# Optimization experiments

Measured on AMD Instinct MI355X. Metric: run time of the kernel, lower is better.

## Reference

```python
import jax, jax.numpy as jnp
import numpy as np

N, M, D = 8192, 8192, 64

def setup_inputs() -> dict:
    key = jax.random.key(0)
    kx, ky = jax.random.split(key)
    x = jax.random.normal(kx, (N, D), dtype=jnp.float32)
    y = jax.random.normal(ky, (M, D), dtype=jnp.float32)
    return {"x": x, "y": y}

def reference(x, y):
    T = 1.0
    # Dmat = 2 - euclidean cdist(x, y), computed via the Gram trick.
    sq = (jnp.sum(x * x, axis=1)[:, None]
          + jnp.sum(y * y, axis=1)[None, :]
          - 2.0 * (x @ y.T))
    Dmat = 2.0 - jnp.sqrt(jnp.maximum(sq, 0.0))          # [N, M]
    logprob_rows = jax.nn.log_softmax(Dmat * T, axis=1)   # [N, M]
    logprob_cols = jax.nn.log_softmax(Dmat.T * T, axis=1) # [M, N]
    choice_rows = jnp.argmax(logprob_rows, axis=1)        # [N]
    choice_cols = jnp.argmax(logprob_cols, axis=1)        # [M]
    seq = jnp.arange(M, dtype=choice_cols.dtype)
    mutual = choice_rows[choice_cols] == seq              # [M] bool
    lp_rows = jnp.take_along_axis(logprob_rows, choice_rows[:, None], axis=1)[:, 0]  # [N]
    lp_cols = jnp.take_along_axis(logprob_cols, choice_cols[:, None], axis=1)[:, 0]  # [M]
    # Padded (jit-friendly) form of the boolean compaction: entries where
    # mutual is False are zeroed; mutual mask identifies valid matches.
    log_probs = jnp.where(mutual, lp_rows[choice_cols] + lp_cols, 0.0)  # [M]
    dmatches = jnp.stack([choice_cols, seq], axis=1)      # [M, 2]
    return (log_probs, dmatches, mutual)
```

## Files before the change

kernel.cpp:

```cpp
#include <hip/hip_runtime.h>
#include <stdint.h>

#define NROWS 8192
#define MCOLS 8192
#define DDIM  64

typedef _Float16 half8   __attribute__((ext_vector_type(8)));
typedef float    floatx4 __attribute__((ext_vector_type(4)));

__device__ __forceinline__ unsigned f2key(float f) {
  unsigned u = __float_as_uint(f);
  return (u & 0x80000000u) ? ~u : (u | 0x80000000u);
}
__device__ __forceinline__ float key2f(unsigned k) {
  unsigned u = (k & 0x80000000u) ? (k & 0x7fffffffu) : ~k;
  return __uint_as_float(u);
}

__global__ void convert_kernel(const float* __restrict__ x, const float* __restrict__ y,
                               _Float16* __restrict__ xh, _Float16* __restrict__ xl,
                               _Float16* __restrict__ yh, _Float16* __restrict__ yl,
                               float* __restrict__ xn, float* __restrict__ yn,
                               unsigned long long* __restrict__ rk,
                               unsigned long long* __restrict__ ck,
                               float* __restrict__ rs, float* __restrict__ cs) {
  const int gid  = blockIdx.x * 256 + threadIdx.x;
  if (gid < NROWS) { rk[gid] = 0ull; rs[gid] = 0.0f; ck[gid] = 0ull; cs[gid] = 0.0f; }

  const int row  = gid >> 6;
  const int k    = threadIdx.x & 63;
  const float* src; _Float16 *dh, *dl; float* nout; int r;
  if (row < NROWS) { src = x; dh = xh; dl = xl; nout = xn; r = row; }
  else             { src = y; dh = yh; dl = yl; nout = yn; r = row - NROWS; }

  float f = src[(size_t)r * DDIM + k];
  _Float16 h = (_Float16)f;
  _Float16 l = (_Float16)((f - (float)h) * 2048.0f);
  int pos = ((r >> 4) << 10) + ((k >> 5) << 9) + ((((k >> 3) & 3) << 4) + (r & 15)) * 8 + (k & 7);
  dh[pos] = h;
  dl[pos] = l;

  float s = f * f;
  #pragma unroll
  for (int off = 32; off > 0; off >>= 1) s += __shfl_down(s, off);
  if (k == 0) nout[r] = s;
}

__global__ __launch_bounds__(256, 4) void mfma_tile_kernel(
    const _Float16* __restrict__ xh, const _Float16* __restrict__ xl,
    const _Float16* __restrict__ yh, const _Float16* __restrict__ yl,
    const float* __restrict__ xn, const float* __restrict__ yn,
    unsigned long long* __restrict__ row_key, float* __restrict__ row_sum,
    unsigned long long* __restrict__ col_key, float* __restrict__ col_sum)
{
  __shared__ unsigned long long lkey[256];
  __shared__ float              lsum[256];

  const int wave = threadIdx.x >> 6;
  const int lane = threadIdx.x & 63;
  const int l15  = lane & 15;
  const int g    = lane >> 4;
  const int ap0  = blockIdx.y * 8 + wave * 2;
  const int ro   = ap0 * 16 + g * 4;
  const int colbase = blockIdx.x * 256;

  lkey[threadIdx.x] = 0ull;
  lsum[threadIdx.x] = 0.0f;
  __syncthreads();

  const half8* xh8 = (const half8*)xh;
  const half8* xl8 = (const half8*)xl;
  const half8* yh8 = (const half8*)yh;
  const half8* yl8 = (const half8*)yl;
  const size_t a0 = (size_t)ap0 * 128 + lane;
  half8 Ah[2][2], Al[2][2];
  #pragma unroll
  for (int p = 0; p < 2; ++p) {
    Ah[p][0] = xh8[a0 + p * 128];      Ah[p][1] = xh8[a0 + p * 128 + 64];
    Al[p][0] = xl8[a0 + p * 128];      Al[p][1] = xl8[a0 + p * 128 + 64];
  }

  float xne[8], rsum[8], rmax[8]; int ridx[8];
  #pragma unroll
  for (int s = 0; s < 8; ++s) {
    xne[s]  = xn[ro + ((s >> 2) << 4) + (s & 3)];
    rsum[s] = 0.0f; rmax[s] = -3.4e38f; ridx[s] = 0;
  }

  const size_t bbase = (size_t)(blockIdx.x * 16) * 128 + lane;
  half8 nbh0 = yh8[bbase], nbh1 = yh8[bbase + 64];
  half8 nbl0 = yl8[bbase], nbl1 = yl8[bbase + 64];

  for (int jt = 0; jt < 16; ++jt) {
    const half8 bh0 = nbh0, bh1 = nbh1, bl0 = nbl0, bl1 = nbl1;
    const int col = colbase + jt * 16 + l15;
    const float ync = yn[col];
    if (jt < 15) {
      const size_t nb = bbase + (size_t)(jt + 1) * 128;
      nbh0 = yh8[nb];  nbh1 = yh8[nb + 64];
      nbl0 = yl8[nb];  nbl1 = yl8[nb + 64];
    }

    float csum = 0.0f, cmax = -3.4e38f; int cs8 = 0;
    #pragma unroll
    for (int p = 0; p < 2; ++p) {
      floatx4 c1 = {}, c2 = {};
      c1 = __builtin_amdgcn_mfma_f32_16x16x32_f16(Ah[p][0], bh0, c1, 0, 0, 0);
      c1 = __builtin_amdgcn_mfma_f32_16x16x32_f16(Ah[p][1], bh1, c1, 0, 0, 0);
      c2 = __builtin_amdgcn_mfma_f32_16x16x32_f16(Al[p][0], bh0, c2, 0, 0, 0);
      c2 = __builtin_amdgcn_mfma_f32_16x16x32_f16(Al[p][1], bh1, c2, 0, 0, 0);
      c2 = __builtin_amdgcn_mfma_f32_16x16x32_f16(Ah[p][0], bl0, c2, 0, 0, 0);
      c2 = __builtin_amdgcn_mfma_f32_16x16x32_f16(Ah[p][1], bl1, c2, 0, 0, 0);
      #pragma unroll
      for (int r = 0; r < 4; ++r) {
        const int s = p * 4 + r;
        float dot = fmaf(c2[r], (1.0f / 2048.0f), c1[r]);
        float sq  = fmaxf(fmaf(-2.0f, dot, xne[s] + ync), 0.0f);
        float d   = 2.0f - __builtin_amdgcn_sqrtf(sq);
        float e   = __expf(d);
        rsum[s] += e;  csum += e;
        if (d > rmax[s]) ridx[s] = col;
        rmax[s] = fmaxf(rmax[s], d);
        if (d > cmax) cs8 = s;
        cmax = fmaxf(cmax, d);
      }
    }

    int crow = ro + ((cs8 >> 2) << 4) + (cs8 & 3);
    unsigned long long ckey =
        ((unsigned long long)f2key(cmax) << 32) | (unsigned long long)(unsigned)(~(unsigned)crow);
    atomicMax(&lkey[jt * 16 + l15], ckey);
    atomicAdd(&lsum[jt * 16 + l15], csum);
  }

  unsigned long long rkk[8];
  #pragma unroll
  for (int s = 0; s < 8; ++s)
    rkk[s] = ((unsigned long long)f2key(rmax[s]) << 32) |
             (unsigned long long)(unsigned)(~(unsigned)ridx[s]);
  #pragma unroll
  for (int off = 1; off < 16; off <<= 1) {
    #pragma unroll
    for (int s = 0; s < 8; ++s) {
      rsum[s] += __shfl_xor(rsum[s], off);
      unsigned long long o = __shfl_xor(rkk[s], off);
      if (o > rkk[s]) rkk[s] = o;
    }
  }
  if (l15 == 0) {
    #pragma unroll
    for (int s = 0; s < 8; ++s) {
      int row = ro + ((s >> 2) << 4) + (s & 3);
      atomicMax(row_key + row, rkk[s]);
      atomicAdd(row_sum + row, rsum[s]);
    }
  }

  __syncthreads();
  {
    int col = colbase + threadIdx.x;
    atomicMax(col_key + col, lkey[threadIdx.x]);
    atomicAdd(col_sum + col, lsum[threadIdx.x]);
  }
}

__global__ void finalize_kernel(const unsigned long long* __restrict__ row_key,
                                const float* __restrict__ row_sum,
                                const unsigned long long* __restrict__ col_key,
                                const float* __restrict__ col_sum,
                                float* __restrict__ out)
{
  int j = blockIdx.x * 256 + threadIdx.x;
  if (j >= MCOLS) return;
  unsigned long long ck = col_key[j];
  int   ci   = (int)(~(unsigned)ck);
  float cmax = key2f((unsigned)(ck >> 32));
  float lp_col = cmax - logf(col_sum[j]);

  unsigned long long rk = row_key[ci];
  int   rj   = (int)(~(unsigned)rk);
  float rmax = key2f((unsigned)(rk >> 32));
  float lp_row = rmax - logf(row_sum[ci]);

  int mut = (rj == j);
  out[j]                 = mut ? (lp_row + lp_col) : 0.0f;
  out[MCOLS + 2 * j + 0] = (float)ci;
  out[MCOLS + 2 * j + 1] = (float)j;
  out[3 * MCOLS + j]     = mut ? 1.0f : 0.0f;
}

extern "C" void kernel_launch(void* const* d_in, const int* in_sizes, int n_in,
                              void* d_out, int out_size, void* d_ws, size_t ws_size,
                              hipStream_t stream) {
  const float* x = (const float*)d_in[0];
  const float* y = (const float*)d_in[1];
  float* out = (float*)d_out;

  char* ws = (char*)d_ws;
  unsigned long long* row_key = (unsigned long long*)(ws);
  unsigned long long* col_key = (unsigned long long*)(ws + 65536);
  float* row_sum = (float*)(ws + 131072);
  float* col_sum = (float*)(ws + 163840);
  float* xn      = (float*)(ws + 196608);
  float* yn      = (float*)(ws + 229376);
  _Float16* xh = (_Float16*)(ws + 262144);
  _Float16* xl = (_Float16*)(ws + 262144 + 1048576);
  _Float16* yh = (_Float16*)(ws + 262144 + 2097152);
  _Float16* yl = (_Float16*)(ws + 262144 + 3145728);

  convert_kernel<<<4096, 256, 0, stream>>>(x, y, xh, xl, yh, yl, xn, yn,
                                           row_key, col_key, row_sum, col_sum);
  dim3 grid(MCOLS / 256, NROWS / 128);
  mfma_tile_kernel<<<grid, 256, 0, stream>>>(xh, xl, yh, yl, xn, yn,
                                             row_key, row_sum, col_key, col_sum);
  finalize_kernel<<<32, 256, 0, stream>>>(row_key, row_sum, col_key, col_sum, out);
}
```

Measured before the change: 129.4 us.

## Fuse fp16 split conversion and norms into the MFMA tile kernel

Removes the separate convert kernel and instead loads fp32 x and y directly inside the tile kernel, splitting them into high/low fp16 parts and computing squared norms in registers with cross-lane shuffles. Workspace zeroing moves to a hipMemsetAsync. This drops one kernel launch and the intermediate global round trip, but every block now redoes the conversion and norm work for its y tiles (64 blocks share each y tile). It also loses the software prefetch of the next B tile, so global load latency is exposed inside the loop.

```diff
diff --git a/kernel.cpp b/kernel.cpp
--- a/kernel.cpp
+++ b/kernel.cpp
@@ -6,6 +6,7 @@
 #define DDIM  64
 
 typedef _Float16 half8   __attribute__((ext_vector_type(8)));
+typedef float    float8  __attribute__((ext_vector_type(8)));
 typedef float    floatx4 __attribute__((ext_vector_type(4)));
 
 __device__ __forceinline__ unsigned f2key(float f) {
@@ -17,39 +18,8 @@
   return __uint_as_float(u);
 }
 
-__global__ void convert_kernel(const float* __restrict__ x, const float* __restrict__ y,
-                               _Float16* __restrict__ xh, _Float16* __restrict__ xl,
-                               _Float16* __restrict__ yh, _Float16* __restrict__ yl,
-                               float* __restrict__ xn, float* __restrict__ yn,
-                               unsigned long long* __restrict__ rk,
-                               unsigned long long* __restrict__ ck,
-                               float* __restrict__ rs, float* __restrict__ cs) {
-  const int gid  = blockIdx.x * 256 + threadIdx.x;
-  if (gid < NROWS) { rk[gid] = 0ull; rs[gid] = 0.0f; ck[gid] = 0ull; cs[gid] = 0.0f; }
-
-  const int row  = gid >> 6;
-  const int k    = threadIdx.x & 63;
-  const float* src; _Float16 *dh, *dl; float* nout; int r;
-  if (row < NROWS) { src = x; dh = xh; dl = xl; nout = xn; r = row; }
-  else             { src = y; dh = yh; dl = yl; nout = yn; r = row - NROWS; }
-
-  float f = src[(size_t)r * DDIM + k];
-  _Float16 h = (_Float16)f;
-  _Float16 l = (_Float16)((f - (float)h) * 2048.0f);
-  int pos = ((r >> 4) << 10) + ((k >> 5) << 9) + ((((k >> 3) & 3) << 4) + (r & 15)) * 8 + (k & 7);
-  dh[pos] = h;
-  dl[pos] = l;
-
-  float s = f * f;
-  #pragma unroll
-  for (int off = 32; off > 0; off >>= 1) s += __shfl_down(s, off);
-  if (k == 0) nout[r] = s;
-}
-
 __global__ __launch_bounds__(256, 4) void mfma_tile_kernel(
-    const _Float16* __restrict__ xh, const _Float16* __restrict__ xl,
-    const _Float16* __restrict__ yh, const _Float16* __restrict__ yl,
-    const float* __restrict__ xn, const float* __restrict__ yn,
+    const float* __restrict__ x, const float* __restrict__ y,
     unsigned long long* __restrict__ row_key, float* __restrict__ row_sum,
     unsigned long long* __restrict__ col_key, float* __restrict__ col_sum)
 {
@@ -59,47 +29,65 @@
   const int wave = threadIdx.x >> 6;
   const int lane = threadIdx.x & 63;
   const int l15  = lane & 15;
-  const int g    = lane >> 4;
+  const int grp  = lane >> 4;
   const int ap0  = blockIdx.y * 8 + wave * 2;
-  const int ro   = ap0 * 16 + g * 4;
+  const int ro   = ap0 * 16 + grp * 4;
   const int colbase = blockIdx.x * 256;
 
   lkey[threadIdx.x] = 0ull;
   lsum[threadIdx.x] = 0.0f;
   __syncthreads();
 
-  const half8* xh8 = (const half8*)xh;
-  const half8* xl8 = (const half8*)xl;
-  const half8* yh8 = (const half8*)yh;
-  const half8* yl8 = (const half8*)yl;
-  const size_t a0 = (size_t)ap0 * 128 + lane;
   half8 Ah[2][2], Al[2][2];
+  float normA[2];
   #pragma unroll
   for (int p = 0; p < 2; ++p) {
-    Ah[p][0] = xh8[a0 + p * 128];      Ah[p][1] = xh8[a0 + p * 128 + 64];
-    Al[p][0] = xl8[a0 + p * 128];      Al[p][1] = xl8[a0 + p * 128 + 64];
+    const float* ax = x + (size_t)((ap0 + p) * 16 + l15) * DDIM + grp * 8;
+    float8 f0 = *(const float8*)ax;
+    float8 f1 = *(const float8*)(ax + 32);
+    float pa = 0.0f;
+    #pragma unroll
+    for (int j = 0; j < 8; ++j) {
+      _Float16 h0 = (_Float16)f0[j];
+      _Float16 h1 = (_Float16)f1[j];
+      Ah[p][0][j] = h0;  Al[p][0][j] = (_Float16)((f0[j] - (float)h0) * 2048.0f);
+      Ah[p][1][j] = h1;  Al[p][1][j] = (_Float16)((f1[j] - (float)h1) * 2048.0f);
+      pa = fmaf(f0[j], f0[j], pa);
+      pa = fmaf(f1[j], f1[j], pa);
+    }
+    pa += __shfl_xor(pa, 16);
+    pa += __shfl_xor(pa, 32);
+    normA[p] = pa;
   }
 
   float xne[8], rsum[8], rmax[8]; int ridx[8];
   #pragma unroll
   for (int s = 0; s < 8; ++s) {
-    xne[s]  = xn[ro + ((s >> 2) << 4) + (s & 3)];
+    xne[s]  = __shfl(normA[s >> 2], grp * 4 + (s & 3));
     rsum[s] = 0.0f; rmax[s] = -3.4e38f; ridx[s] = 0;
   }
 
-  const size_t bbase = (size_t)(blockIdx.x * 16) * 128 + lane;
-  half8 nbh0 = yh8[bbase], nbh1 = yh8[bbase + 64];
-  half8 nbl0 = yl8[bbase], nbl1 = yl8[bbase + 64];
-
   for (int jt = 0; jt < 16; ++jt) {
-    const half8 bh0 = nbh0, bh1 = nbh1, bl0 = nbl0, bl1 = nbl1;
+    const int cpg = blockIdx.x * 16 + jt;
+    const float* by = y + (size_t)(cpg * 16 + l15) * DDIM + grp * 8;
+    float8 g0 = *(const float8*)by;
+    float8 g1 = *(const float8*)(by + 32);
+
+    half8 bh0, bh1, bl0, bl1;
+    float pb = 0.0f;
+    #pragma unroll
+    for (int j = 0; j < 8; ++j) {
+      _Float16 h0 = (_Float16)g0[j];
+      _Float16 h1 = (_Float16)g1[j];
+      bh0[j] = h0;  bl0[j] = (_Float16)((g0[j] - (float)h0) * 2048.0f);
+      bh1[j] = h1;  bl1[j] = (_Float16)((g1[j] - (float)h1) * 2048.0f);
+      pb = fmaf(g0[j], g0[j], pb);
+      pb = fmaf(g1[j], g1[j], pb);
+    }
+    pb += __shfl_xor(pb, 16);
+    pb += __shfl_xor(pb, 32);
+    const float ync = pb;
     const int col = colbase + jt * 16 + l15;
-    const float ync = yn[col];
-    if (jt < 15) {
-      const size_t nb = bbase + (size_t)(jt + 1) * 128;
-      nbh0 = yh8[nb];  nbh1 = yh8[nb + 64];
-      nbl0 = yl8[nb];  nbl1 = yl8[nb + 64];
-    }
 
     float csum = 0.0f, cmax = -3.4e38f; int cs8 = 0;
     #pragma unroll
@@ -128,7 +116,8 @@
 
     int crow = ro + ((cs8 >> 2) << 4) + (cs8 & 3);
     unsigned long long ckey =
-        ((unsigned long long)f2key(cmax) << 32) | (unsigned long long)(unsigned)(~(unsigned)crow);
+        ((unsigned long long)f2key(cmax) << 32) |
+        (unsigned long long)(unsigned)(~(unsigned)crow);
     atomicMax(&lkey[jt * 16 + l15], ckey);
     atomicAdd(&lsum[jt * 16 + l15], csum);
   }
@@ -201,17 +190,11 @@
   unsigned long long* col_key = (unsigned long long*)(ws + 65536);
   float* row_sum = (float*)(ws + 131072);
   float* col_sum = (float*)(ws + 163840);
-  float* xn      = (float*)(ws + 196608);
-  float* yn      = (float*)(ws + 229376);
-  _Float16* xh = (_Float16*)(ws + 262144);
-  _Float16* xl = (_Float16*)(ws + 262144 + 1048576);
-  _Float16* yh = (_Float16*)(ws + 262144 + 2097152);
-  _Float16* yl = (_Float16*)(ws + 262144 + 3145728);
-
-  convert_kernel<<<4096, 256, 0, stream>>>(x, y, xh, xl, yh, yl, xn, yn,
-                                           row_key, col_key, row_sum, col_sum);
+
+  hipMemsetAsync(ws, 0, 196608, stream);
+
   dim3 grid(MCOLS / 256, NROWS / 128);
-  mfma_tile_kernel<<<grid, 256, 0, stream>>>(xh, xl, yh, yl, xn, yn,
-                                             row_key, row_sum, col_key, col_sum);
+  mfma_tile_kernel<<<grid, 256, 0, stream>>>(x, y, row_key, row_sum,
+                                             col_key, col_sum);
   finalize_kernel<<<32, 256, 0, stream>>>(row_key, row_sum, col_key, col_sum, out);
 }
```

New measurement: 141.5 us. 1.09x slower.
